# Optimization experiments

Hardware: AMD Instinct MI355X
Metric: run time of the kernel (lower is better)

## Reference

```python
import jax, jax.numpy as jnp
import numpy as np

B, C, H, W = 8, 256, 64, 64
HEADS, FFN = 4, 2048


def setup_inputs() -> dict:
    key = jax.random.key(0)
    ks = jax.random.split(key, 5)
    s = lambda k, shape, scale: (jax.random.normal(k, shape, jnp.float32) * scale)
    return dict(
        x=jax.random.normal(ks[0], (B, C, H, W), jnp.float32),
        w_qkv=s(ks[1], (3 * C, C), 0.02), b_qkv=jnp.zeros((3 * C,), jnp.float32),
        w_proj=s(ks[2], (C, C), 0.02), b_proj=jnp.zeros((C,), jnp.float32),
        w_ffn1=s(ks[3], (FFN, C), 0.02), b_ffn1=jnp.zeros((FFN,), jnp.float32),
        w_ffn2=s(ks[4], (C, FFN), 0.02), b_ffn2=jnp.zeros((C,), jnp.float32),
        g1=jnp.ones((C,), jnp.float32), be1=jnp.zeros((C,), jnp.float32),
        g2=jnp.ones((C,), jnp.float32), be2=jnp.zeros((C,), jnp.float32),
    )


def _ln(x, g, b):
    # LayerNorm over last axis (channels), biased variance, eps=1e-5 (torch default)
    mu = x.mean(-1, keepdims=True)
    var = x.var(-1, keepdims=True)
    return (x - mu) * jax.lax.rsqrt(var + 1e-5) * g + b


def reference(x, w_qkv, b_qkv, w_proj, b_proj, w_ffn1, b_ffn1, w_ffn2, b_ffn2,
              g1, be1, g2, be2):
    Bx, Cx, Hx, Wx = x.shape
    h = HEADS
    d = Cx // h
    N = Hx * Wx
    # pre-LN over channel dim (applied on (B, N, C))
    xt = x.reshape(Bx, Cx, N).transpose(0, 2, 1)          # (B, N, C)
    x_ln = _ln(xt, g1, be1)
    # 1x1-conv QKV == per-pixel linear
    qkv = x_ln @ w_qkv.T + b_qkv                          # (B, N, 3C)
    q, k, v = jnp.split(qkv, 3, axis=-1)
    rh = lambda t: t.transpose(0, 2, 1).reshape(Bx, h, d, N)  # (B, h, d, N)
    qh = rh(q) / jnp.sqrt(jnp.float32(d))
    kh = rh(k)
    vh = rh(v)
    # NOTE: faithful to source einsum — attention over channel (head_dim) axes,
    # contracting over spatial N. attn is (B, h, d, d).
    attn = jax.nn.softmax(jnp.einsum('bhdn,bhen->bhde', qh, kh), axis=-1)
    out = jnp.einsum('bhde,bhen->bhdn', attn, vh).reshape(Bx, Cx, N)
    out = out.transpose(0, 2, 1) @ w_proj.T + b_proj      # (B, N, C)
    out = _ln(out, g2, be2)
    out = jax.nn.relu(out @ w_ffn1.T + b_ffn1) @ w_ffn2.T + b_ffn2
    return out.transpose(0, 2, 1).reshape(Bx, Cx, Hx, Wx) + x
```

## Files before the change

### kernel.cpp

```cpp
#include <hip/hip_runtime.h>
#include <stdint.h>

typedef unsigned short u16;
typedef __attribute__((ext_vector_type(8))) short bf16x8;
typedef __attribute__((ext_vector_type(4))) float f32x4;

__device__ __forceinline__ u16 f2b(float f) {
  uint32_t x = __builtin_bit_cast(uint32_t, f);
  uint32_t r = (x + 0x7FFFu + ((x >> 16) & 1u)) >> 16;
  return (u16)r;
}
__device__ __forceinline__ float b2f(u16 u) {
  return __builtin_bit_cast(float, ((uint32_t)u) << 16);
}

__device__ __forceinline__ void gload16(const u16* g, u16* l) {
  __builtin_amdgcn_global_load_lds(
      (const __attribute__((address_space(1))) uint32_t*)g,
      (__attribute__((address_space(3))) uint32_t*)l, 16, 0, 0);
}

__global__ __launch_bounds__(256) void cvt_bf16(const float* __restrict__ in,
                                                u16* __restrict__ out, int n) {
  int i = (blockIdx.x * 256 + threadIdx.x) * 4;
  if (i + 3 < n) {
    float4 f = *(const float4*)(in + i);
    ushort4 u;
    u.x = f2b(f.x); u.y = f2b(f.y); u.z = f2b(f.z); u.w = f2b(f.w);
    *(ushort4*)(out + i) = u;
  }
}

__global__ __launch_bounds__(256)
void ln1_transpose(const float* __restrict__ x, const float* __restrict__ g,
                   const float* __restrict__ be, u16* __restrict__ xln) {
  int b = blockIdx.x >> 6;
  int n0 = (blockIdx.x & 63) << 6;
  int t = threadIdx.x;
  int w = t >> 6, l = t & 63;
  const float* xb = x + (size_t)b * 256 * 4096 + n0;
  __shared__ float red[8][64];
  __shared__ float mu[64], rs[64];
  __shared__ u16 tile[256][65];
  float s = 0.f, ss = 0.f;
#pragma unroll 8
  for (int i = 0; i < 64; ++i) {
    int c = (w << 6) + i;
    float v = xb[(size_t)c * 4096 + l];
    s += v; ss += v * v;
    tile[c][l] = f2b(v);
  }
  red[w][l] = s;
  red[4 + w][l] = ss;
  __syncthreads();
  if (t < 64) {
    float S = red[0][t] + red[1][t] + red[2][t] + red[3][t];
    float SS = red[4][t] + red[5][t] + red[6][t] + red[7][t];
    float m = S * 0.00390625f;
    float var = SS * 0.00390625f - m * m;
    mu[t] = m;
    rs[t] = rsqrtf(var + 1e-5f);
  }
  __syncthreads();
  int c4 = l << 2;
  float g0 = g[c4], gA = g[c4 + 1], gB = g[c4 + 2], gC = g[c4 + 3];
  float e0 = be[c4], eA = be[c4 + 1], eB = be[c4 + 2], eC = be[c4 + 3];
  u16* orow = xln + ((size_t)(b * 4096 + n0)) * 256 + c4;
#pragma unroll
  for (int jj = 0; jj < 16; ++jj) {
    int pp = (jj << 2) + w;
    float m = mu[pp], r = rs[pp];
    ushort4 o;
    o.x = f2b((b2f(tile[c4 + 0][pp]) - m) * r * g0 + e0);
    o.y = f2b((b2f(tile[c4 + 1][pp]) - m) * r * gA + eA);
    o.z = f2b((b2f(tile[c4 + 2][pp]) - m) * r * gB + eB);
    o.w = f2b((b2f(tile[c4 + 3][pp]) - m) * r * gC + eC);
    *(ushort4*)(orow + (size_t)pp * 256) = o;
  }
}

__global__ __launch_bounds__(256)
void gemm_bt(const u16* __restrict__ A, const u16* __restrict__ B,
             const float* __restrict__ bias, u16* __restrict__ C,
             int N, int K, int relu) {
  __shared__ u16 As[2][128 * 32];
  __shared__ u16 Bs[2][128 * 32];
  int t = threadIdx.x;
  int lane = t & 63, wid = t >> 6;
  int tm = blockIdx.y << 7, tn = blockIdx.x << 7;
  int wm = (wid >> 1) << 6, wn = (wid & 1) << 6;
  int fr = lane & 15, fk = (lane >> 4) << 3;
  f32x4 acc[4][4];
#pragma unroll
  for (int i = 0; i < 4; ++i)
#pragma unroll
    for (int j = 0; j < 4; ++j) acc[i][j] = (f32x4){0.f, 0.f, 0.f, 0.f};

  int sr = t >> 2, sc = (t & 3) << 3;
  const u16* Ag = A + (size_t)(tm + sr) * K + sc;
  const u16* Bg = B + (size_t)(tn + sr) * K + sc;
  size_t rstep = (size_t)64 * K;
  int wo = wid * 512;

  gload16(Ag, As[0] + wo);
  gload16(Ag + rstep, As[0] + wo + 2048);
  gload16(Bg, Bs[0] + wo);
  gload16(Bg + rstep, Bs[0] + wo + 2048);
  __syncthreads();

  int buf = 0;
  for (int k0 = 0; k0 < K; k0 += 32) {
    if (k0 + 32 < K) {
      int nb = buf ^ 1;
      gload16(Ag + k0 + 32, As[nb] + wo);
      gload16(Ag + k0 + 32 + rstep, As[nb] + wo + 2048);
      gload16(Bg + k0 + 32, Bs[nb] + wo);
      gload16(Bg + k0 + 32 + rstep, Bs[nb] + wo + 2048);
    }
    bf16x8 af[4], bf[4];
#pragma unroll
    for (int mi = 0; mi < 4; ++mi)
      af[mi] = *(const bf16x8*)&As[buf][(wm + mi * 16 + fr) * 32 + fk];
#pragma unroll
    for (int ni = 0; ni < 4; ++ni)
      bf[ni] = *(const bf16x8*)&Bs[buf][(wn + ni * 16 + fr) * 32 + fk];
#pragma unroll
    for (int mi = 0; mi < 4; ++mi)
#pragma unroll
      for (int ni = 0; ni < 4; ++ni)
        acc[mi][ni] = __builtin_amdgcn_mfma_f32_16x16x32_bf16(
            af[mi], bf[ni], acc[mi][ni], 0, 0, 0);
    __syncthreads();
    buf ^= 1;
  }

  int rbase = (lane >> 4) << 2;
#pragma unroll
  for (int mi = 0; mi < 4; ++mi) {
#pragma unroll
    for (int ni = 0; ni < 4; ++ni) {
      int col = tn + wn + ni * 16 + fr;
      float bv = bias[col];
#pragma unroll
      for (int r = 0; r < 4; ++r) {
        float v = acc[mi][ni][r] + bv;
        if (relu) v = fmaxf(v, 0.f);
        C[(size_t)(tm + wm + mi * 16 + rbase + r) * N + col] = f2b(v);
      }
    }
  }
}

__global__ __launch_bounds__(256)
void attn_s(const u16* __restrict__ qkv, float* __restrict__ Sp) {
  int kc = blockIdx.x, bh = blockIdx.y;
  int b = bh >> 2, h = bh & 3;
  int t = threadIdx.x, lane = t & 63, w = t >> 6;
  int fr = lane & 15, fkg = (lane >> 4) << 3;
  const u16* base = qkv + (size_t)b * 4096 * 768;
  int d0 = w << 4;
  f32x4 acc[4];
#pragma unroll
  for (int i = 0; i < 4; ++i) acc[i] = (f32x4){0.f, 0.f, 0.f, 0.f};
  int nbase = kc * 512;
  for (int ks = 0; ks < 16; ++ks) {
    int n = nbase + ks * 32 + fkg;
    const u16* qp = base + (size_t)n * 768 + h * 64;
    const u16* kp = qp + 256;
    bf16x8 aq;
#pragma unroll
    for (int j = 0; j < 8; ++j) aq[j] = (short)qp[(size_t)j * 768 + d0 + fr];
#pragma unroll
    for (int ni = 0; ni < 4; ++ni) {
      bf16x8 bk;
#pragma unroll
      for (int j = 0; j < 8; ++j) bk[j] = (short)kp[(size_t)j * 768 + ni * 16 + fr];
      acc[ni] = __builtin_amdgcn_mfma_f32_16x16x32_bf16(aq, bk, acc[ni], 0, 0, 0);
    }
  }
  float* out = Sp + (size_t)(bh * 8 + kc) * 64 * 64;
  int dr = d0 + ((lane >> 4) << 2);
#pragma unroll
  for (int ni = 0; ni < 4; ++ni)
#pragma unroll
    for (int r = 0; r < 4; ++r)
      out[(dr + r) * 64 + ni * 16 + fr] = acc[ni][r] * 0.125f;
}

__global__ __launch_bounds__(256)
void attn_softmax(const float* __restrict__ Sp, u16* __restrict__ attn) {
  int bh = blockIdx.x;
  int t = threadIdx.x;
  int d = t >> 2, q = t & 3;
  const float* sp = Sp + (size_t)bh * 8 * 64 * 64;
  float v[16];
#pragma unroll
  for (int i = 0; i < 16; ++i) v[i] = 0.f;
  for (int kc = 0; kc < 8; ++kc) {
    const float* p = sp + kc * 4096 + d * 64 + q * 16;
#pragma unroll
    for (int i = 0; i < 16; i += 4) {
      float4 f = *(const float4*)(p + i);
      v[i] += f.x; v[i + 1] += f.y; v[i + 2] += f.z; v[i + 3] += f.w;
    }
  }
  float m = v[0];
#pragma unroll
  for (int i = 1; i < 16; ++i) m = fmaxf(m, v[i]);
  m = fmaxf(m, __shfl_xor(m, 1));
  m = fmaxf(m, __shfl_xor(m, 2));
  float s = 0.f;
#pragma unroll
  for (int i = 0; i < 16; ++i) { v[i] = expf(v[i] - m); s += v[i]; }
  s += __shfl_xor(s, 1);
  s += __shfl_xor(s, 2);
  float inv = 1.f / s;
  u16* out = attn + (size_t)bh * 4096 + d * 64 + q * 16;
#pragma unroll
  for (int i = 0; i < 16; i += 4) {
    ushort4 u;
    u.x = f2b(v[i] * inv); u.y = f2b(v[i + 1] * inv);
    u.z = f2b(v[i + 2] * inv); u.w = f2b(v[i + 3] * inv);
    *(ushort4*)(out + i) = u;
  }
}

__global__ __launch_bounds__(256)
void attn_av(const u16* __restrict__ qkv, const u16* __restrict__ attn,
             u16* __restrict__ attnout) {
  int nt = blockIdx.x, bh = blockIdx.y;
  int b = bh >> 2, h = bh & 3;
  int t = threadIdx.x, lane = t & 63, w = t >> 6;
  int fr = lane & 15, fk = (lane >> 4) << 3;
  int n0 = nt * 128 + w * 32;
  const u16* vg = qkv + (size_t)b * 4096 * 768 + 512 + h * 64;
  const u16* at = attn + (size_t)bh * 4096;
  f32x4 acc[2][4];
#pragma unroll
  for (int i = 0; i < 2; ++i)
#pragma unroll
    for (int j = 0; j < 4; ++j) acc[i][j] = (f32x4){0.f, 0.f, 0.f, 0.f};
#pragma unroll
  for (int kk = 0; kk < 2; ++kk) {
    bf16x8 av[2], bv[4];
#pragma unroll
    for (int mi = 0; mi < 2; ++mi)
      av[mi] = *(const bf16x8*)(vg + (size_t)(n0 + mi * 16 + fr) * 768 + kk * 32 + fk);
#pragma unroll
    for (int ni = 0; ni < 4; ++ni)
      bv[ni] = *(const bf16x8*)(at + (size_t)(ni * 16 + fr) * 64 + kk * 32 + fk);
#pragma unroll
    for (int mi = 0; mi < 2; ++mi)
#pragma unroll
      for (int ni = 0; ni < 4; ++ni)
        acc[mi][ni] = __builtin_amdgcn_mfma_f32_16x16x32_bf16(
            av[mi], bv[ni], acc[mi][ni], 0, 0, 0);
  }
  u16* outp = attnout + (size_t)b * 4096 * 256 + h * 64;
  int rbase = (lane >> 4) << 2;
#pragma unroll
  for (int mi = 0; mi < 2; ++mi)
#pragma unroll
    for (int ni = 0; ni < 4; ++ni)
#pragma unroll
      for (int r = 0; r < 4; ++r)
        outp[(size_t)(n0 + mi * 16 + rbase + r) * 256 + ni * 16 + fr] =
            f2b(acc[mi][ni][r]);
}

__global__ __launch_bounds__(256)
void ln2_rows(u16* __restrict__ io, const float* __restrict__ g,
              const float* __restrict__ be) {
  int w = threadIdx.x >> 6, lane = threadIdx.x & 63;
  size_t row = (size_t)blockIdx.x * 4 + w;
  u16* p = io + row * 256 + lane * 4;
  ushort4 u = *(ushort4*)p;
  float v0 = b2f(u.x), v1 = b2f(u.y), v2 = b2f(u.z), v3 = b2f(u.w);
  float s = v0 + v1 + v2 + v3;
  float ss = v0 * v0 + v1 * v1 + v2 * v2 + v3 * v3;
#pragma unroll
  for (int off = 1; off < 64; off <<= 1) {
    s += __shfl_xor(s, off);
    ss += __shfl_xor(ss, off);
  }
  float m = s * 0.00390625f;
  float var = ss * 0.00390625f - m * m;
  float r = rsqrtf(var + 1e-5f);
  int c = lane * 4;
  u.x = f2b((v0 - m) * r * g[c] + be[c]);
  u.y = f2b((v1 - m) * r * g[c + 1] + be[c + 1]);
  u.z = f2b((v2 - m) * r * g[c + 2] + be[c + 2]);
  u.w = f2b((v3 - m) * r * g[c + 3] + be[c + 3]);
  *(ushort4*)p = u;
}

__global__ __launch_bounds__(256)
void resid_transpose(const u16* __restrict__ f2o, const float* __restrict__ x,
                     float* __restrict__ out) {
  int blk = blockIdx.x;
  int b = blk >> 8;
  int ct = (blk >> 6) & 3, ntl = blk & 63;
  int c0 = ct << 6, n0 = ntl << 6;
  int t = threadIdx.x;
  __shared__ float ldsT[64][65];
  {
    int n = t >> 2, cq = (t & 3) << 4;
    const u16* src = f2o + (size_t)(b * 4096 + n0 + n) * 256 + c0 + cq;
    union { uint4 v[2]; u16 s[16]; } tmp;
    tmp.v[0] = *(const uint4*)src;
    tmp.v[1] = *(const uint4*)(src + 8);
#pragma unroll
    for (int i = 0; i < 16; ++i) ldsT[cq + i][n] = b2f(tmp.s[i]);
  }
  __syncthreads();
  const float* xb = x + (size_t)b * 256 * 4096;
  float* ob = out + (size_t)b * 256 * 4096;
  int l = t & 63;
#pragma unroll
  for (int i = 0; i < 16; ++i) {
    int c = i * 4 + (t >> 6);
    size_t idx = (size_t)(c0 + c) * 4096 + n0 + l;
    ob[idx] = ldsT[c][l] + xb[idx];
  }
}

extern "C" void kernel_launch(void* const* d_in, const int* in_sizes, int n_in,
                              void* d_out, int out_size, void* d_ws, size_t ws_size,
                              hipStream_t stream) {
  (void)in_sizes; (void)n_in; (void)out_size;
  const float* x      = (const float*)d_in[0];
  const float* w_qkv  = (const float*)d_in[1];
  const float* b_qkv  = (const float*)d_in[2];
  const float* w_proj = (const float*)d_in[3];
  const float* b_proj = (const float*)d_in[4];
  const float* w_ffn1 = (const float*)d_in[5];
  const float* b_ffn1 = (const float*)d_in[6];
  const float* w_ffn2 = (const float*)d_in[7];
  const float* b_ffn2 = (const float*)d_in[8];
  const float* g1  = (const float*)d_in[9];
  const float* be1 = (const float*)d_in[10];
  const float* g2  = (const float*)d_in[11];
  const float* be2 = (const float*)d_in[12];

  u16* p = (u16*)d_ws;
  u16* wq = p;       p += 196608;
  u16* wp = p;       p += 65536;
  u16* w1 = p;       p += 524288;
  u16* w2 = p;       p += 524288;
  u16* xln = p;      p += (size_t)32768 * 256;
  u16* qkv = p;      p += (size_t)32768 * 768;
  u16* attnw = p;    p += 32 * 64 * 64;
  u16* attnout = p;  p += (size_t)32768 * 256;
  u16* projout = p;  p += (size_t)32768 * 256;
  u16* ffn2 = p;     p += (size_t)32768 * 256;
  float* Sp = (float*)p; p += (size_t)2 * 32 * 8 * 64 * 64;
  u16* ffn1 = p;

  size_t fixed = (size_t)(p - (u16*)d_ws);
  int nc = 4;
  if (ws_size >= (fixed + (size_t)32768 * 2048) * 2) nc = 1;
  else if (ws_size >= (fixed + (size_t)16384 * 2048) * 2) nc = 2;
  int Mc = 32768 / nc;

  cvt_bf16<<<192, 256, 0, stream>>>(w_qkv, wq, 196608);
  cvt_bf16<<<64, 256, 0, stream>>>(w_proj, wp, 65536);
  cvt_bf16<<<512, 256, 0, stream>>>(w_ffn1, w1, 524288);
  cvt_bf16<<<512, 256, 0, stream>>>(w_ffn2, w2, 524288);

  ln1_transpose<<<512, 256, 0, stream>>>(x, g1, be1, xln);

  gemm_bt<<<dim3(6, 256), 256, 0, stream>>>(xln, wq, b_qkv, qkv, 768, 256, 0);

  attn_s<<<dim3(8, 32), 256, 0, stream>>>(qkv, Sp);
  attn_softmax<<<32, 256, 0, stream>>>(Sp, attnw);
  attn_av<<<dim3(32, 32), 256, 0, stream>>>(qkv, attnw, attnout);

  gemm_bt<<<dim3(2, 256), 256, 0, stream>>>(attnout, wp, b_proj, projout, 256, 256, 0);
  ln2_rows<<<8192, 256, 0, stream>>>(projout, g2, be2);

  for (int mc = 0; mc < nc; ++mc) {
    gemm_bt<<<dim3(16, Mc / 128), 256, 0, stream>>>(
        projout + (size_t)mc * Mc * 256, w1, b_ffn1, ffn1, 2048, 256, 1);
    gemm_bt<<<dim3(2, Mc / 128), 256, 0, stream>>>(
        ffn1, w2, b_ffn2, ffn2 + (size_t)mc * Mc * 256, 256, 2048, 0);
  }

  resid_transpose<<<2048, 256, 0, stream>>>(ffn2, x, (float*)d_out);
}
```

Before: 330.6 us.

## Triple-buffer GEMM LDS staging with explicit vmcnt waits and split barriers

Changes the bf16 GEMM's shared-memory staging from double to triple buffering. Loads are issued two tiles ahead, and explicit s_waitcnt vmcnt counts wait only for the oldest tile. Fragments are read into registers before a second barrier, so the next global-to-LDS load can overwrite the freed buffer while the MFMAs run. This aims to hide global latency better, at the cost of more LDS (48KB per block), which may reduce occupancy, and of fragile hand-tuned waitcnt values.

Result: no change. 326.1 us (-1.4%).

```diff
diff --git a/kernel.cpp b/kernel.cpp
--- a/kernel.cpp
+++ b/kernel.cpp
@@ -83,8 +83,8 @@
 void gemm_bt(const u16* __restrict__ A, const u16* __restrict__ B,
              const float* __restrict__ bias, u16* __restrict__ C,
              int N, int K, int relu) {
-  __shared__ u16 As[2][128 * 32];
-  __shared__ u16 Bs[2][128 * 32];
+  __shared__ u16 As[3][128 * 32];
+  __shared__ u16 Bs[3][128 * 32];
   int t = threadIdx.x;
   int lane = t & 63, wid = t >> 6;
   int tm = blockIdx.y << 7, tn = blockIdx.x << 7;
@@ -102,21 +102,29 @@
   size_t rstep = (size_t)64 * K;
   int wo = wid * 512;
 
-  gload16(Ag, As[0] + wo);
-  gload16(Ag + rstep, As[0] + wo + 2048);
-  gload16(Bg, Bs[0] + wo);
-  gload16(Bg + rstep, Bs[0] + wo + 2048);
-  __syncthreads();
+#define STAGE(kt, bi)                                    \
+  do {                                                   \
+    int off_ = (kt) << 5;                                \
+    gload16(Ag + off_, As[bi] + wo);                     \
+    gload16(Ag + off_ + rstep, As[bi] + wo + 2048);      \
+    gload16(Bg + off_, Bs[bi] + wo);                     \
+    gload16(Bg + off_ + rstep, Bs[bi] + wo + 2048);      \
+  } while (0)
+
+  int nk = K >> 5;
+  STAGE(0, 0);
+  STAGE(1, 1);
+  STAGE(2, 2);
 
   int buf = 0;
-  for (int k0 = 0; k0 < K; k0 += 32) {
-    if (k0 + 32 < K) {
-      int nb = buf ^ 1;
-      gload16(Ag + k0 + 32, As[nb] + wo);
-      gload16(Ag + k0 + 32 + rstep, As[nb] + wo + 2048);
-      gload16(Bg + k0 + 32, Bs[nb] + wo);
-      gload16(Bg + k0 + 32 + rstep, Bs[nb] + wo + 2048);
-    }
+  for (int k = 0; k < nk; ++k) {
+    int rem = nk - 1 - k;
+    if (rem >= 2)      asm volatile("s_waitcnt vmcnt(8)" ::: "memory");
+    else if (rem == 1) asm volatile("s_waitcnt vmcnt(4)" ::: "memory");
+    else               asm volatile("s_waitcnt vmcnt(0)" ::: "memory");
+    __builtin_amdgcn_s_barrier();
+    __builtin_amdgcn_sched_barrier(0);
+
     bf16x8 af[4], bf[4];
 #pragma unroll
     for (int mi = 0; mi < 4; ++mi)
@@ -124,15 +132,24 @@
 #pragma unroll
     for (int ni = 0; ni < 4; ++ni)
       bf[ni] = *(const bf16x8*)&Bs[buf][(wn + ni * 16 + fr) * 32 + fk];
+
+    asm volatile("s_waitcnt lgkmcnt(0)" ::: "memory");
+    __builtin_amdgcn_sched_barrier(0);
+    __builtin_amdgcn_s_barrier();
+    __builtin_amdgcn_sched_barrier(0);
+
+    if (k + 3 < nk) STAGE(k + 3, buf);
+
 #pragma unroll
     for (int mi = 0; mi < 4; ++mi)
 #pragma unroll
       for (int ni = 0; ni < 4; ++ni)
         acc[mi][ni] = __builtin_amdgcn_mfma_f32_16x16x32_bf16(
             af[mi], bf[ni], acc[mi][ni], 0, 0, 0);
-    __syncthreads();
-    buf ^= 1;
-  }
+
+    buf = (buf == 2) ? 0 : buf + 1;
+  }
+#undef STAGE
 
   int rbase = (lane >> 4) << 2;
 #pragma unroll
```
